# Optimization experiments

Hardware: AMD Instinct MI355X
Metric: run time of the kernel (lower is better)

The kernel has to match this reference:

```python
import jax, jax.numpy as jnp
import numpy as np
from jax import lax

B, C, H, W = 4, 64, 64, 64
CH = C // 2  # edge_detect hidden channels
BN_EPS = 1e-5


def conv1x1(x, w, b):
    # x: (B,C,H,W), w: (O,C), b: (O,)
    return jnp.einsum('bchw,oc->bohw', x, w) + b[None, :, None, None]


def setup_inputs() -> dict:
    key = jax.random.key(0)
    ks = jax.random.split(key, 12)
    s = 1.0 / np.sqrt(C)
    inp = {
        'x': jax.random.normal(ks[0], (B, C, H, W), jnp.float32),
        'Wq': jax.random.normal(ks[1], (C, C), jnp.float32) * s,
        'bq': jnp.zeros((C,), jnp.float32),
        'Wk': jax.random.normal(ks[2], (C, C), jnp.float32) * s,
        'bk': jnp.zeros((C,), jnp.float32),
        'Wv': jax.random.normal(ks[3], (C, C), jnp.float32) * s,
        'bv': jnp.zeros((C,), jnp.float32),
        'We1': jax.random.normal(ks[4], (CH, C, 3, 3), jnp.float32) * (1.0 / np.sqrt(C * 9)),
        'be1': jnp.zeros((CH,), jnp.float32),
        'bn_w': jnp.ones((CH,), jnp.float32),
        'bn_b': jnp.zeros((CH,), jnp.float32),
        'bn_mean': jnp.zeros((CH,), jnp.float32),
        'bn_var': jnp.ones((CH,), jnp.float32),
        'We2': jax.random.normal(ks[5], (1, CH), jnp.float32) * (1.0 / np.sqrt(CH)),
        'be2': jnp.zeros((1,), jnp.float32),
        'gamma': jax.random.normal(ks[6], (1,), jnp.float32) * 0.1,
        'beta': jax.random.normal(ks[7], (1,), jnp.float32) * 0.1,
    }
    return inp


def reference(x, Wq, bq, Wk, bk, Wv, bv, We1, be1, bn_w, bn_b, bn_mean, bn_var, We2, be2, gamma, beta):
    b, c, h, w = x.shape
    hw = h * w
    q = conv1x1(x, Wq, bq).reshape(b, c, hw).transpose(0, 2, 1)  # (B,HW,C)
    k = conv1x1(x, Wk, bk).reshape(b, c, hw)                      # (B,C,HW)
    v = conv1x1(x, Wv, bv).reshape(b, c, hw)                      # (B,C,HW)

    energy = jnp.einsum('bnc,bcm->bnm', q, k)                      # (B,HW,HW)
    attention = jax.nn.softmax(energy, axis=-1)

    # edge_detect: 3x3 conv -> BN (eval stats) -> ReLU -> 1x1 conv -> sigmoid
    e = lax.conv_general_dilated(x, We1, (1, 1), 'SAME',
                                 dimension_numbers=('NCHW', 'OIHW', 'NCHW'))
    e = e + be1[None, :, None, None]
    e = (e - bn_mean[None, :, None, None]) * jax.lax.rsqrt(bn_var + BN_EPS)[None, :, None, None]
    e = e * bn_w[None, :, None, None] + bn_b[None, :, None, None]
    e = jax.nn.relu(e)
    e = conv1x1(e, We2, be2)                                       # (B,1,H,W)
    edge = jax.nn.sigmoid(e).reshape(b, 1, hw)                     # (B,1,HW)

    fa = attention * (1.0 + beta[0] * edge)                        # broadcast over query dim
    denom = jnp.maximum(jnp.sum(jnp.abs(fa), axis=2, keepdims=True), 1e-12)
    fa = fa / denom                                                # L1 renorm along keys

    out = jnp.einsum('bcm,bnm->bcn', v, fa).reshape(b, c, h, w)
    return gamma[0] * out + x
```

## Files before the change

kernel.cpp:

```cpp
#include <hip/hip_runtime.h>
#include <hip/hip_bf16.h>

typedef unsigned short u16;
typedef __attribute__((ext_vector_type(8))) __bf16 bf16x8;
typedef __attribute__((ext_vector_type(4))) float f32x4;


__device__ __forceinline__ u16 f2bf(float f) {
    unsigned u = __builtin_bit_cast(unsigned, f);
    u += 0x7FFFu + ((u >> 16) & 1u);
    return (u16)(u >> 16);
}
__device__ __forceinline__ float bf2f(u16 v) {
    unsigned u = ((unsigned)v) << 16;
    return __builtin_bit_cast(float, u);
}

__global__ __launch_bounds__(256) void qkv_edge_kernel(
    const float* __restrict__ x,
    const float* __restrict__ Wq, const float* __restrict__ bq,
    const float* __restrict__ Wk, const float* __restrict__ bk,
    const float* __restrict__ Wv, const float* __restrict__ bv,
    const float* __restrict__ We1, const float* __restrict__ be1,
    const float* __restrict__ bn_w, const float* __restrict__ bn_b,
    const float* __restrict__ bn_mean, const float* __restrict__ bn_var,
    const float* __restrict__ We2, const float* __restrict__ be2,
    const float* __restrict__ beta,
    u16* __restrict__ Qt, u16* __restrict__ Kt, u16* __restrict__ Vm,
    float* __restrict__ wkey)
{
    __shared__ __align__(16) u16 sm[33280];
    const int t = threadIdx.x;
    const int wv = t >> 6, lane = t & 63;
    const int quad = lane >> 4, l15 = lane & 15;

    if (blockIdx.x < 256) {
        u16* Wl   = sm;
        u16* xt_s = sm + 13824;
        u16* vt   = sm + 13824 + 4224;
        const int b = blockIdx.x >> 6;
        const int n0 = (blockIdx.x & 63) << 6;

        const float* Wmat[3] = {Wq, Wk, Wv};
#pragma unroll
        for (int m = 0; m < 3; ++m)
#pragma unroll
            for (int i = 0; i < 4; ++i) {
                int u = t + i * 256;
                float4 w4 = *reinterpret_cast<const float4*>(Wmat[m] + u * 4);
                int row = u >> 4, col = (u & 15) * 4;
                uint2 pk;
                pk.x = (unsigned)f2bf(w4.x) | ((unsigned)f2bf(w4.y) << 16);
                pk.y = (unsigned)f2bf(w4.z) | ((unsigned)f2bf(w4.w) << 16);
                *reinterpret_cast<uint2*>(&Wl[(m * 64 + row) * 72 + col]) = pk;
            }
        for (int i = 0; i < 16; ++i) {
            int lin = t + i * 256;
            int c = lin >> 6, nn = lin & 63;
            xt_s[nn * 66 + c] = f2bf(x[(size_t)(b * 64 + c) * 4096 + n0 + nn]);
        }
        __syncthreads();

        bf16x8 bx[2];
#pragma unroll
        for (int h = 0; h < 2; ++h)
            bx[h] = *reinterpret_cast<const bf16x8*>(
                &xt_s[(wv * 16 + l15) * 66 + h * 32 + quad * 8]);

        f32x4 d[3][4];
#pragma unroll
        for (int m = 0; m < 3; ++m)
#pragma unroll
            for (int mt = 0; mt < 4; ++mt) d[m][mt] = (f32x4){0.f, 0.f, 0.f, 0.f};

#pragma unroll
        for (int h = 0; h < 2; ++h)
#pragma unroll
            for (int m = 0; m < 3; ++m)
#pragma unroll
                for (int mt = 0; mt < 4; ++mt) {
                    bf16x8 af = *reinterpret_cast<const bf16x8*>(
                        &Wl[(m * 64 + mt * 16 + l15) * 72 + h * 32 + quad * 8]);
                    d[m][mt] = __builtin_amdgcn_mfma_f32_16x16x32_bf16(af, bx[h], d[m][mt], 0, 0, 0);
                }

        const float* bias[3] = {bq, bk, bv};
        const float L2E = 1.44269504f;
#pragma unroll
        for (int m = 0; m < 3; ++m)
#pragma unroll
            for (int mt = 0; mt < 4; ++mt) {
                float4 bi = *reinterpret_cast<const float4*>(bias[m] + mt * 16 + quad * 4);
                d[m][mt][0] += bi.x; d[m][mt][1] += bi.y; d[m][mt][2] += bi.z; d[m][mt][3] += bi.w;
                if (m == 0) {
                    d[m][mt][0] *= L2E; d[m][mt][1] *= L2E;
                    d[m][mt][2] *= L2E; d[m][mt][3] *= L2E;
                }
            }

        const int rowchunk = (n0 >> 4) + wv;
#pragma unroll
        for (int m = 0; m < 2; ++m) {
            u16* base = (m == 0 ? Qt : Kt) + (size_t)b * 262144;
#pragma unroll
            for (int mt = 0; mt < 4; ++mt) {
                uint2 pk;
                pk.x = (unsigned)f2bf(d[m][mt][0]) | ((unsigned)f2bf(d[m][mt][1]) << 16);
                pk.y = (unsigned)f2bf(d[m][mt][2]) | ((unsigned)f2bf(d[m][mt][3]) << 16);
                *reinterpret_cast<uint2*>(
                    base + ((size_t)(rowchunk * 8 + mt * 2 + (quad >> 1))) * 128 +
                    l15 * 8 + (quad & 1) * 4) = pk;
            }
        }
#pragma unroll
        for (int mt = 0; mt < 4; ++mt)
#pragma unroll
            for (int r = 0; r < 4; ++r)
                vt[(mt * 16 + quad * 4 + r) * 72 + wv * 16 + l15] = f2bf(d[2][mt][r]);
        __syncthreads();
        {
            u16* Vb_st = Vm + (size_t)b * 262144;
            const int kt = n0 >> 6;
#pragma unroll
            for (int i = 0; i < 2; ++i) {
                int unit = t + i * 256;
                int f = unit >> 7, hq = (unit >> 4) & 7, cl = unit & 15;
                const u16* src = &vt[(f * 16 + cl) * 72 + hq * 8];
                uint4 v4 = *reinterpret_cast<const uint4*>(src);
                *reinterpret_cast<uint4*>(
                    Vb_st + ((size_t)((kt * 4 + f) * 8 + hq)) * 128 + cl * 8) = v4;
            }
        }
    } else {
        u16* Ae_s = sm;
        u16* xr_s = sm + 18688;
        const int eb = blockIdx.x - 256;
        const int b = eb >> 6, h = eb & 63;

        if (t < 192) {
            int kh = t / 64, rem = t & 63;
            int col = (rem >> 5) * 65, ci2 = (rem & 31) * 2;
            *reinterpret_cast<unsigned*>(&xr_s[(kh * 66 + col) * 72 + ci2]) = 0u;
        }
#pragma unroll
        for (int i = 0; i < 18; ++i) {
            int u = t + i * 256;
            int ch = u / 144;
            int rem = u - ch * 144;
            int p = rem >> 4, cig = (rem & 15) * 4;
            const float* src = We1 + ch * 576 + cig * 9 + p;
            float a = src[0], b2 = src[9], c2 = src[18], d2 = src[27];
            uint2 pk;
            pk.x = (unsigned)f2bf(a) | ((unsigned)f2bf(b2) << 16);
            pk.y = (unsigned)f2bf(c2) | ((unsigned)f2bf(d2) << 16);
            *reinterpret_cast<uint2*>(&Ae_s[ch * 584 + p * 64 + cig]) = pk;
        }
#pragma unroll
        for (int i = 0; i < 12; ++i) {
            int u = t + i * 256;
            int w = u & 63, cig = (u >> 6) & 15, kh = u >> 10;
            int hs = h + kh - 1;
            float v0 = 0.f, v1 = 0.f, v2 = 0.f, v3 = 0.f;
            if ((unsigned)hs < 64u) {
                const float* src = x + ((size_t)(b * 64 + cig * 4) * 64 + hs) * 64 + w;
                v0 = src[0]; v1 = src[4096]; v2 = src[8192]; v3 = src[12288];
            }
            uint2 pk;
            pk.x = (unsigned)f2bf(v0) | ((unsigned)f2bf(v1) << 16);
            pk.y = (unsigned)f2bf(v2) | ((unsigned)f2bf(v3) << 16);
            *reinterpret_cast<uint2*>(&xr_s[(kh * 66 + w + 1) * 72 + cig * 4]) = pk;
        }
        __syncthreads();

        f32x4 e[2];
        e[0] = (f32x4){0.f, 0.f, 0.f, 0.f};
        e[1] = (f32x4){0.f, 0.f, 0.f, 0.f};
#pragma unroll
        for (int p = 0; p < 9; ++p) {
            const int kh = p / 3, kw = p - kh * 3;
#pragma unroll
            for (int half = 0; half < 2; ++half) {
                bf16x8 bfr = *reinterpret_cast<const bf16x8*>(
                    &xr_s[(kh * 66 + wv * 16 + l15 + kw) * 72 + half * 32 + quad * 8]);
#pragma unroll
                for (int mt = 0; mt < 2; ++mt) {
                    bf16x8 af = *reinterpret_cast<const bf16x8*>(
                        &Ae_s[(mt * 16 + l15) * 584 + p * 64 + half * 32 + quad * 8]);
                    e[mt] = __builtin_amdgcn_mfma_f32_16x16x32_bf16(af, bfr, e[mt], 0, 0, 0);
                }
            }
        }
        float partial = 0.f;
#pragma unroll
        for (int mt = 0; mt < 2; ++mt) {
            float4 bw = *reinterpret_cast<const float4*>(bn_w    + mt * 16 + quad * 4);
            float4 bb = *reinterpret_cast<const float4*>(bn_b    + mt * 16 + quad * 4);
            float4 bm = *reinterpret_cast<const float4*>(bn_mean + mt * 16 + quad * 4);
            float4 bv2 = *reinterpret_cast<const float4*>(bn_var + mt * 16 + quad * 4);
            float4 b1 = *reinterpret_cast<const float4*>(be1     + mt * 16 + quad * 4);
            float4 w2 = *reinterpret_cast<const float4*>(We2     + mt * 16 + quad * 4);
            float sc, sh;
            sc = bw.x * rsqrtf(bv2.x + 1e-5f); sh = (b1.x - bm.x) * sc + bb.x;
            partial += fmaxf(e[mt][0] * sc + sh, 0.f) * w2.x;
            sc = bw.y * rsqrtf(bv2.y + 1e-5f); sh = (b1.y - bm.y) * sc + bb.y;
            partial += fmaxf(e[mt][1] * sc + sh, 0.f) * w2.y;
            sc = bw.z * rsqrtf(bv2.z + 1e-5f); sh = (b1.z - bm.z) * sc + bb.z;
            partial += fmaxf(e[mt][2] * sc + sh, 0.f) * w2.z;
            sc = bw.w * rsqrtf(bv2.w + 1e-5f); sh = (b1.w - bm.w) * sc + bb.w;
            partial += fmaxf(e[mt][3] * sc + sh, 0.f) * w2.w;
        }
        partial += __shfl_xor(partial, 16);
        partial += __shfl_xor(partial, 32);
        if (lane < 16) {
            float s = partial + be2[0];
            float sg = 1.f / (1.f + __expf(-s));
            wkey[(size_t)b * 4096 + h * 64 + wv * 16 + lane] = 1.f + beta[0] * sg;
        }
    }
}

template <int NSPLIT>
__global__ __launch_bounds__(128, 4) void attn_kernel(
    const u16* __restrict__ Qt, const u16* __restrict__ Kt,
    const u16* __restrict__ Vm, const float* __restrict__ wkey,
    u16* __restrict__ O_part, float* __restrict__ l_part)
{
    constexpr int KT_ITERS = 64 / NSPLIT;
    __shared__ __align__(16) u16 p_s_all[2 * 32 * 68];
    const int t = threadIdx.x;
    const int qi = blockIdx.x / NSPLIT;
    const int split = blockIdx.x % NSPLIT;
    const int b = qi >> 6;
    const int n0 = (qi & 63) << 6;
    const int wv = t >> 6, lane = t & 63;
    const int quad = lane >> 4, l15 = lane & 15;
    u16* p_s = p_s_all + wv * (32 * 68);

    const u16* Qb = Qt + (size_t)b * 262144;
    const u16* Kb = Kt + (size_t)b * 262144;
    const u16* Vb = Vm + (size_t)b * 262144;
    const float* wb = wkey + (size_t)b * 4096;

    bf16x8 qf[2][2];
#pragma unroll
    for (int nt = 0; nt < 2; ++nt)
#pragma unroll
        for (int h = 0; h < 2; ++h)
            qf[nt][h] = __builtin_bit_cast(bf16x8, *reinterpret_cast<const uint4*>(
                Qb + ((size_t)(((n0 >> 4) + wv * 2 + nt) * 8 + h * 4 + quad)) * 128 + l15 * 8));

    const int kt0 = split * KT_ITERS;
    uint4 kf[4][2];
    float4 wf[4];
#pragma unroll
    for (int mt = 0; mt < 4; ++mt) {
#pragma unroll
        for (int h = 0; h < 2; ++h)
            kf[mt][h] = *reinterpret_cast<const uint4*>(
                Kb + ((size_t)((kt0 * 4 + mt) * 8 + h * 4 + quad)) * 128 + l15 * 8);
        wf[mt] = *reinterpret_cast<const float4*>(wb + kt0 * 64 + mt * 16 + quad * 4);
    }

    const uint4 ones_u = {0x3F803F80u, 0x3F803F80u, 0x3F803F80u, 0x3F803F80u};
    const bf16x8 onesf = __builtin_bit_cast(bf16x8, ones_u);

    f32x4 o[2][4];
    f32x4 l5[2];
#pragma unroll
    for (int m2 = 0; m2 < 2; ++m2) {
#pragma unroll
        for (int f = 0; f < 4; ++f) o[m2][f] = (f32x4){0.f, 0.f, 0.f, 0.f};
        l5[m2] = (f32x4){0.f, 0.f, 0.f, 0.f};
    }

    for (int kt = kt0; kt < kt0 + KT_ITERS; ++kt) {
        uint4 vf[4][2];
#pragma unroll
        for (int f = 0; f < 4; ++f)
#pragma unroll
            for (int h = 0; h < 2; ++h)
                vf[f][h] = *reinterpret_cast<const uint4*>(
                    Vb + ((size_t)((kt * 4 + f) * 8 + h * 4 + quad)) * 128 + l15 * 8);

        f32x4 s[4][2];
#pragma unroll
        for (int mt = 0; mt < 4; ++mt)
#pragma unroll
            for (int nt = 0; nt < 2; ++nt) {
                f32x4 a = (f32x4){0.f, 0.f, 0.f, 0.f};
                a = __builtin_amdgcn_mfma_f32_16x16x32_bf16(
                        __builtin_bit_cast(bf16x8, kf[mt][0]), qf[nt][0], a, 0, 0, 0);
                a = __builtin_amdgcn_mfma_f32_16x16x32_bf16(
                        __builtin_bit_cast(bf16x8, kf[mt][1]), qf[nt][1], a, 0, 0, 0);
                s[mt][nt] = a;
            }

        const int ktn = (kt + 1 < kt0 + KT_ITERS) ? kt + 1 : kt0;
#pragma unroll
        for (int mt = 0; mt < 4; ++mt)
#pragma unroll
            for (int h = 0; h < 2; ++h)
                kf[mt][h] = *reinterpret_cast<const uint4*>(
                    Kb + ((size_t)((ktn * 4 + mt) * 8 + h * 4 + quad)) * 128 + l15 * 8);

        const float OFF = 17.3123405f;
#pragma unroll
        for (int mt = 0; mt < 4; ++mt) {
            const float* wfp = reinterpret_cast<const float*>(&wf[mt]);
#pragma unroll
            for (int nt = 0; nt < 2; ++nt) {
                float p0 = exp2f(s[mt][nt][0] - OFF) * wfp[0];
                float p1 = exp2f(s[mt][nt][1] - OFF) * wfp[1];
                float p2 = exp2f(s[mt][nt][2] - OFF) * wfp[2];
                float p3 = exp2f(s[mt][nt][3] - OFF) * wfp[3];
                unsigned u0 = __builtin_bit_cast(unsigned, p0);
                unsigned u1 = __builtin_bit_cast(unsigned, p1);
                unsigned u2 = __builtin_bit_cast(unsigned, p2);
                unsigned u3 = __builtin_bit_cast(unsigned, p3);
                uint2 packed;
                packed.x = (u0 >> 16) | (u1 & 0xFFFF0000u);
                packed.y = (u2 >> 16) | (u3 & 0xFFFF0000u);
                *reinterpret_cast<uint2*>(
                    &p_s[(nt * 16 + l15) * 68 + mt * 16 + quad * 4]) = packed;
            }
        }

#pragma unroll
        for (int mt = 0; mt < 4; ++mt)
            wf[mt] = *reinterpret_cast<const float4*>(wb + ktn * 64 + mt * 16 + quad * 4);

        bf16x8 pa[2][2];
#pragma unroll
        for (int m2 = 0; m2 < 2; ++m2)
#pragma unroll
            for (int h = 0; h < 2; ++h) {
                uint2 lo = *reinterpret_cast<const uint2*>(
                    &p_s[(m2 * 16 + l15) * 68 + h * 32 + quad * 8]);
                uint2 hi = *reinterpret_cast<const uint2*>(
                    &p_s[(m2 * 16 + l15) * 68 + h * 32 + quad * 8 + 4]);
                uint4 c4; c4.x = lo.x; c4.y = lo.y; c4.z = hi.x; c4.w = hi.y;
                pa[m2][h] = __builtin_bit_cast(bf16x8, c4);
            }

#pragma unroll
        for (int m2 = 0; m2 < 2; ++m2) {
#pragma unroll
            for (int f = 0; f < 4; ++f) {
                o[m2][f] = __builtin_amdgcn_mfma_f32_16x16x32_bf16(
                    pa[m2][0], __builtin_bit_cast(bf16x8, vf[f][0]), o[m2][f], 0, 0, 0);
                o[m2][f] = __builtin_amdgcn_mfma_f32_16x16x32_bf16(
                    pa[m2][1], __builtin_bit_cast(bf16x8, vf[f][1]), o[m2][f], 0, 0, 0);
            }
            l5[m2] = __builtin_amdgcn_mfma_f32_16x16x32_bf16(pa[m2][0], onesf, l5[m2], 0, 0, 0);
            l5[m2] = __builtin_amdgcn_mfma_f32_16x16x32_bf16(pa[m2][1], onesf, l5[m2], 0, 0, 0);
        }
    }

    const size_t pbase = (size_t)blockIdx.x * 4096;
#pragma unroll
    for (int m2 = 0; m2 < 2; ++m2) {
        if (l15 == 0) {
            float4 lv;
            lv.x = l5[m2][0]; lv.y = l5[m2][1]; lv.z = l5[m2][2]; lv.w = l5[m2][3];
            *reinterpret_cast<float4*>(
                &l_part[(size_t)blockIdx.x * 64 + wv * 32 + m2 * 16 + quad * 4]) = lv;
        }
#pragma unroll
        for (int f = 0; f < 4; ++f) {
            uint2 pk;
            pk.x = (unsigned)f2bf(o[m2][f][0]) | ((unsigned)f2bf(o[m2][f][1]) << 16);
            pk.y = (unsigned)f2bf(o[m2][f][2]) | ((unsigned)f2bf(o[m2][f][3]) << 16);
            *reinterpret_cast<uint2*>(
                &O_part[pbase + ((((wv * 2 + m2) * 4 + f) * 4 + quad)) * 64 + l15 * 4]) = pk;
        }
    }
}

template <int NSPLIT>
__global__ __launch_bounds__(256) void combine_kernel(
    const u16* __restrict__ O_part, const float* __restrict__ l_part,
    const float* __restrict__ x, const float* __restrict__ g_gamma,
    float* __restrict__ out)
{
    __shared__ float ot[64 * 65];
    __shared__ float ls[64];
    const int t = threadIdx.x;
    const int qi = blockIdx.x;
    const int b = qi >> 6;
    const int n0 = (qi & 63) << 6;
    const int f = t >> 6, quad = (t >> 4) & 3, l15 = t & 15;
    const float gamma = g_gamma[0];

    float acc[2][2][4];
#pragma unroll
    for (int wv = 0; wv < 2; ++wv)
#pragma unroll
        for (int m2 = 0; m2 < 2; ++m2)
#pragma unroll
            for (int r = 0; r < 4; ++r) acc[wv][m2][r] = 0.f;

#pragma unroll
    for (int s4 = 0; s4 < NSPLIT; ++s4) {
        const u16* base = O_part + ((size_t)(qi * NSPLIT + s4)) * 4096;
#pragma unroll
        for (int wv = 0; wv < 2; ++wv)
#pragma unroll
            for (int m2 = 0; m2 < 2; ++m2) {
                uint2 u = *reinterpret_cast<const uint2*>(
                    base + ((((wv * 2 + m2) * 4 + f) * 4 + quad)) * 64 + l15 * 4);
                acc[wv][m2][0] += bf2f((u16)(u.x & 0xFFFF));
                acc[wv][m2][1] += bf2f((u16)(u.x >> 16));
                acc[wv][m2][2] += bf2f((u16)(u.y & 0xFFFF));
                acc[wv][m2][3] += bf2f((u16)(u.y >> 16));
            }
    }
#pragma unroll
    for (int wv = 0; wv < 2; ++wv)
#pragma unroll
        for (int m2 = 0; m2 < 2; ++m2)
#pragma unroll
            for (int r = 0; r < 4; ++r)
                ot[(wv * 32 + m2 * 16 + quad * 4 + r) * 65 + f * 16 + l15] = acc[wv][m2][r];
    if (t < 64) {
        float lsum = 0.f;
#pragma unroll
        for (int s4 = 0; s4 < NSPLIT; ++s4)
            lsum += l_part[((size_t)(qi * NSPLIT + s4)) * 64 + t];
        ls[t] = gamma / fmaxf(lsum, 1e-30f);
    }
    __syncthreads();
    {
        const int c = t >> 2, nseg = t & 3;
        const size_t gbase = ((size_t)(b * 64 + c)) * 4096 + n0 + nseg * 16;
#pragma unroll
        for (int j = 0; j < 4; ++j) {
            float4 xv = *reinterpret_cast<const float4*>(&x[gbase + j * 4]);
            float4 rv;
            int nl = nseg * 16 + j * 4;
            rv.x = ot[(nl + 0) * 65 + c] * ls[nl + 0] + xv.x;
            rv.y = ot[(nl + 1) * 65 + c] * ls[nl + 1] + xv.y;
            rv.z = ot[(nl + 2) * 65 + c] * ls[nl + 2] + xv.z;
            rv.w = ot[(nl + 3) * 65 + c] * ls[nl + 3] + xv.w;
            *reinterpret_cast<float4*>(&out[gbase + j * 4]) = rv;
        }
    }
}

extern "C" void kernel_launch(void* const* d_in, const int* in_sizes, int n_in,
                              void* d_out, int out_size, void* d_ws, size_t ws_size,
                              hipStream_t stream) {
    const float* x      = (const float*)d_in[0];
    const float* Wq     = (const float*)d_in[1];
    const float* bq     = (const float*)d_in[2];
    const float* Wk     = (const float*)d_in[3];
    const float* bk     = (const float*)d_in[4];
    const float* Wv     = (const float*)d_in[5];
    const float* bv     = (const float*)d_in[6];
    const float* We1    = (const float*)d_in[7];
    const float* be1    = (const float*)d_in[8];
    const float* bn_w   = (const float*)d_in[9];
    const float* bn_b   = (const float*)d_in[10];
    const float* bn_mean= (const float*)d_in[11];
    const float* bn_var = (const float*)d_in[12];
    const float* We2    = (const float*)d_in[13];
    const float* be2    = (const float*)d_in[14];
    const float* gamma  = (const float*)d_in[15];
    const float* beta   = (const float*)d_in[16];

    char* ws = (char*)d_ws;
    const size_t KB = 1024, MB = 1024 * 1024;
    u16*   Qt     = (u16*)ws;
    u16*   Kt     = (u16*)(ws + 2 * MB);
    u16*   Vm     = (u16*)(ws + 4 * MB);
    float* wkey   = (float*)(ws + 6 * MB);
    float* l_part = (float*)(ws + 6 * MB + 64 * KB);
    u16*   O_part = (u16*)(ws + 6 * MB + 576 * KB);

    const bool use8 = ws_size >= (6 * MB + 576 * KB + (size_t)2048 * 64 * 64 * 2);

    float* out = (float*)d_out;

    qkv_edge_kernel<<<dim3(512), dim3(256), 0, stream>>>(
        x, Wq, bq, Wk, bk, Wv, bv, We1, be1, bn_w, bn_b, bn_mean, bn_var,
        We2, be2, beta, Qt, Kt, Vm, wkey);
    if (use8) {
        attn_kernel<8><<<dim3(2048), dim3(128), 0, stream>>>(Qt, Kt, Vm, wkey, O_part, l_part);
        combine_kernel<8><<<dim3(256), dim3(256), 0, stream>>>(O_part, l_part, x, gamma, out);
    } else {
        attn_kernel<4><<<dim3(1024), dim3(128), 0, stream>>>(Qt, Kt, Vm, wkey, O_part, l_part);
        combine_kernel<4><<<dim3(256), dim3(256), 0, stream>>>(O_part, l_part, x, gamma, out);
    }
}
```

Baseline: 148.6 us.

## Pass softmax probabilities via lane shuffles instead of LDS and transpose PV MFMA

Replaces the LDS round trip that moved the probability tile into the A-operand layout with cross-lane shuffles. The PV product is transposed so V becomes the A operand and P the B operand, which changes the accumulator layout and the row-sum output indexing. The combine kernel's shared-memory tile is adjusted to match, now written with float4 stores and a padded stride of 68. Launch bounds drop from 4 to 2 blocks per SIMD, allowing more registers but possibly lowering occupancy; the shuffles also add many cross-lane instructions per iteration.

```diff
diff --git a/kernel.cpp b/kernel.cpp
--- a/kernel.cpp
+++ b/kernel.cpp
@@ -220,13 +220,12 @@
 }
 
 template <int NSPLIT>
-__global__ __launch_bounds__(128, 4) void attn_kernel(
+__global__ __launch_bounds__(128, 2) void attn_kernel(
     const u16* __restrict__ Qt, const u16* __restrict__ Kt,
     const u16* __restrict__ Vm, const float* __restrict__ wkey,
     u16* __restrict__ O_part, float* __restrict__ l_part)
 {
     constexpr int KT_ITERS = 64 / NSPLIT;
-    __shared__ __align__(16) u16 p_s_all[2 * 32 * 68];
     const int t = threadIdx.x;
     const int qi = blockIdx.x / NSPLIT;
     const int split = blockIdx.x % NSPLIT;
@@ -234,7 +233,10 @@
     const int n0 = (qi & 63) << 6;
     const int wv = t >> 6, lane = t & 63;
     const int quad = lane >> 4, l15 = lane & 15;
-    u16* p_s = p_s_all + wv * (32 * 68);
+
+    const int src0 = ((quad & 1) * 2) * 16 + l15;
+    const int src1 = src0 + 16;
+    const bool msel = (quad >> 1) != 0;
 
     const u16* Qb = Qt + (size_t)b * 262144;
     const u16* Kb = Kt + (size_t)b * 262144;
@@ -264,14 +266,14 @@
     const uint4 ones_u = {0x3F803F80u, 0x3F803F80u, 0x3F803F80u, 0x3F803F80u};
     const bf16x8 onesf = __builtin_bit_cast(bf16x8, ones_u);
 
-    f32x4 o[2][4];
+    f32x4 o[4][2];
     f32x4 l5[2];
 #pragma unroll
-    for (int m2 = 0; m2 < 2; ++m2) {
-#pragma unroll
-        for (int f = 0; f < 4; ++f) o[m2][f] = (f32x4){0.f, 0.f, 0.f, 0.f};
-        l5[m2] = (f32x4){0.f, 0.f, 0.f, 0.f};
-    }
+    for (int fc = 0; fc < 4; ++fc)
+#pragma unroll
+        for (int nt = 0; nt < 2; ++nt) o[fc][nt] = (f32x4){0.f, 0.f, 0.f, 0.f};
+#pragma unroll
+    for (int nt = 0; nt < 2; ++nt) l5[nt] = (f32x4){0.f, 0.f, 0.f, 0.f};
 
     for (int kt = kt0; kt < kt0 + KT_ITERS; ++kt) {
         uint4 vf[4][2];
@@ -303,6 +305,7 @@
                 kf[mt][h] = *reinterpret_cast<const uint4*>(
                     Kb + ((size_t)((ktn * 4 + mt) * 8 + h * 4 + quad)) * 128 + l15 * 8);
 
+        uint2 pk[4][2];
         const float OFF = 17.3123405f;
 #pragma unroll
         for (int mt = 0; mt < 4; ++mt) {
@@ -317,11 +320,8 @@
                 unsigned u1 = __builtin_bit_cast(unsigned, p1);
                 unsigned u2 = __builtin_bit_cast(unsigned, p2);
                 unsigned u3 = __builtin_bit_cast(unsigned, p3);
-                uint2 packed;
-                packed.x = (u0 >> 16) | (u1 & 0xFFFF0000u);
-                packed.y = (u2 >> 16) | (u3 & 0xFFFF0000u);
-                *reinterpret_cast<uint2*>(
-                    &p_s[(nt * 16 + l15) * 68 + mt * 16 + quad * 4]) = packed;
+                pk[mt][nt].x = (u0 >> 16) | (u1 & 0xFFFF0000u);
+                pk[mt][nt].y = (u2 >> 16) | (u3 & 0xFFFF0000u);
             }
         }
 
@@ -329,49 +329,53 @@
         for (int mt = 0; mt < 4; ++mt)
             wf[mt] = *reinterpret_cast<const float4*>(wb + ktn * 64 + mt * 16 + quad * 4);
 
-        bf16x8 pa[2][2];
-#pragma unroll
-        for (int m2 = 0; m2 < 2; ++m2)
-#pragma unroll
-            for (int h = 0; h < 2; ++h) {
-                uint2 lo = *reinterpret_cast<const uint2*>(
-                    &p_s[(m2 * 16 + l15) * 68 + h * 32 + quad * 8]);
-                uint2 hi = *reinterpret_cast<const uint2*>(
-                    &p_s[(m2 * 16 + l15) * 68 + h * 32 + quad * 8 + 4]);
-                uint4 c4; c4.x = lo.x; c4.y = lo.y; c4.z = hi.x; c4.w = hi.y;
-                pa[m2][h] = __builtin_bit_cast(bf16x8, c4);
-            }
-
-#pragma unroll
-        for (int m2 = 0; m2 < 2; ++m2) {
-#pragma unroll
-            for (int f = 0; f < 4; ++f) {
-                o[m2][f] = __builtin_amdgcn_mfma_f32_16x16x32_bf16(
-                    pa[m2][0], __builtin_bit_cast(bf16x8, vf[f][0]), o[m2][f], 0, 0, 0);
-                o[m2][f] = __builtin_amdgcn_mfma_f32_16x16x32_bf16(
-                    pa[m2][1], __builtin_bit_cast(bf16x8, vf[f][1]), o[m2][f], 0, 0, 0);
-            }
-            l5[m2] = __builtin_amdgcn_mfma_f32_16x16x32_bf16(pa[m2][0], onesf, l5[m2], 0, 0, 0);
-            l5[m2] = __builtin_amdgcn_mfma_f32_16x16x32_bf16(pa[m2][1], onesf, l5[m2], 0, 0, 0);
+        bf16x8 pb[2][2];
+#pragma unroll
+        for (int h = 0; h < 2; ++h)
+#pragma unroll
+            for (int nt = 0; nt < 2; ++nt) {
+                unsigned a0x = (unsigned)__shfl((int)pk[h * 2][nt].x, src0, 64);
+                unsigned a1x = (unsigned)__shfl((int)pk[h * 2 + 1][nt].x, src0, 64);
+                unsigned a0y = (unsigned)__shfl((int)pk[h * 2][nt].y, src0, 64);
+                unsigned a1y = (unsigned)__shfl((int)pk[h * 2 + 1][nt].y, src0, 64);
+                unsigned a0z = (unsigned)__shfl((int)pk[h * 2][nt].x, src1, 64);
+                unsigned a1z = (unsigned)__shfl((int)pk[h * 2 + 1][nt].x, src1, 64);
+                unsigned a0w = (unsigned)__shfl((int)pk[h * 2][nt].y, src1, 64);
+                unsigned a1w = (unsigned)__shfl((int)pk[h * 2 + 1][nt].y, src1, 64);
+                uint4 g;
+                g.x = msel ? a1x : a0x;
+                g.y = msel ? a1y : a0y;
+                g.z = msel ? a1z : a0z;
+                g.w = msel ? a1w : a0w;
+                pb[nt][h] = __builtin_bit_cast(bf16x8, g);
+            }
+
+#pragma unroll
+        for (int nt = 0; nt < 2; ++nt) {
+#pragma unroll
+            for (int fc = 0; fc < 4; ++fc) {
+                o[fc][nt] = __builtin_amdgcn_mfma_f32_16x16x32_bf16(
+                    __builtin_bit_cast(bf16x8, vf[fc][0]), pb[nt][0], o[fc][nt], 0, 0, 0);
+                o[fc][nt] = __builtin_amdgcn_mfma_f32_16x16x32_bf16(
+                    __builtin_bit_cast(bf16x8, vf[fc][1]), pb[nt][1], o[fc][nt], 0, 0, 0);
+            }
+            l5[nt] = __builtin_amdgcn_mfma_f32_16x16x32_bf16(onesf, pb[nt][0], l5[nt], 0, 0, 0);
+            l5[nt] = __builtin_amdgcn_mfma_f32_16x16x32_bf16(onesf, pb[nt][1], l5[nt], 0, 0, 0);
         }
     }
 
     const size_t pbase = (size_t)blockIdx.x * 4096;
 #pragma unroll
-    for (int m2 = 0; m2 < 2; ++m2) {
-        if (l15 == 0) {
-            float4 lv;
-            lv.x = l5[m2][0]; lv.y = l5[m2][1]; lv.z = l5[m2][2]; lv.w = l5[m2][3];
-            *reinterpret_cast<float4*>(
-                &l_part[(size_t)blockIdx.x * 64 + wv * 32 + m2 * 16 + quad * 4]) = lv;
-        }
-#pragma unroll
-        for (int f = 0; f < 4; ++f) {
-            uint2 pk;
-            pk.x = (unsigned)f2bf(o[m2][f][0]) | ((unsigned)f2bf(o[m2][f][1]) << 16);
-            pk.y = (unsigned)f2bf(o[m2][f][2]) | ((unsigned)f2bf(o[m2][f][3]) << 16);
+    for (int nt = 0; nt < 2; ++nt) {
+        if (quad == 0)
+            l_part[(size_t)blockIdx.x * 64 + wv * 32 + nt * 16 + l15] = l5[nt][0];
+#pragma unroll
+        for (int fc = 0; fc < 4; ++fc) {
+            uint2 pk2;
+            pk2.x = (unsigned)f2bf(o[fc][nt][0]) | ((unsigned)f2bf(o[fc][nt][1]) << 16);
+            pk2.y = (unsigned)f2bf(o[fc][nt][2]) | ((unsigned)f2bf(o[fc][nt][3]) << 16);
             *reinterpret_cast<uint2*>(
-                &O_part[pbase + ((((wv * 2 + m2) * 4 + f) * 4 + quad)) * 64 + l15 * 4]) = pk;
+                &O_part[pbase + ((((wv * 2 + nt) * 4 + fc) * 4 + quad)) * 64 + l15 * 4]) = pk2;
         }
     }
 }
@@ -382,7 +386,7 @@
     const float* __restrict__ x, const float* __restrict__ g_gamma,
     float* __restrict__ out)
 {
-    __shared__ float ot[64 * 65];
+    __shared__ float ot[64 * 68];
     __shared__ float ls[64];
     const int t = threadIdx.x;
     const int qi = blockIdx.x;
@@ -395,9 +399,9 @@
 #pragma unroll
     for (int wv = 0; wv < 2; ++wv)
 #pragma unroll
-        for (int m2 = 0; m2 < 2; ++m2)
-#pragma unroll
-            for (int r = 0; r < 4; ++r) acc[wv][m2][r] = 0.f;
+        for (int nt = 0; nt < 2; ++nt)
+#pragma unroll
+            for (int r = 0; r < 4; ++r) acc[wv][nt][r] = 0.f;
 
 #pragma unroll
     for (int s4 = 0; s4 < NSPLIT; ++s4) {
@@ -405,22 +409,25 @@
 #pragma unroll
         for (int wv = 0; wv < 2; ++wv)
 #pragma unroll
-            for (int m2 = 0; m2 < 2; ++m2) {
+            for (int nt = 0; nt < 2; ++nt) {
                 uint2 u = *reinterpret_cast<const uint2*>(
-                    base + ((((wv * 2 + m2) * 4 + f) * 4 + quad)) * 64 + l15 * 4);
-                acc[wv][m2][0] += bf2f((u16)(u.x & 0xFFFF));
-                acc[wv][m2][1] += bf2f((u16)(u.x >> 16));
-                acc[wv][m2][2] += bf2f((u16)(u.y & 0xFFFF));
-                acc[wv][m2][3] += bf2f((u16)(u.y >> 16));
+                    base + ((((wv * 2 + nt) * 4 + f) * 4 + quad)) * 64 + l15 * 4);
+                acc[wv][nt][0] += bf2f((u16)(u.x & 0xFFFF));
+                acc[wv][nt][1] += bf2f((u16)(u.x >> 16));
+                acc[wv][nt][2] += bf2f((u16)(u.y & 0xFFFF));
+                acc[wv][nt][3] += bf2f((u16)(u.y >> 16));
             }
     }
 #pragma unroll
     for (int wv = 0; wv < 2; ++wv)
 #pragma unroll
-        for (int m2 = 0; m2 < 2; ++m2)
-#pragma unroll
-            for (int r = 0; r < 4; ++r)
-                ot[(wv * 32 + m2 * 16 + quad * 4 + r) * 65 + f * 16 + l15] = acc[wv][m2][r];
+        for (int nt = 0; nt < 2; ++nt) {
+            float4 v4;
+            v4.x = acc[wv][nt][0]; v4.y = acc[wv][nt][1];
+            v4.z = acc[wv][nt][2]; v4.w = acc[wv][nt][3];
+            *reinterpret_cast<float4*>(
+                &ot[(wv * 32 + nt * 16 + l15) * 68 + f * 16 + quad * 4]) = v4;
+        }
     if (t < 64) {
         float lsum = 0.f;
 #pragma unroll
@@ -437,10 +444,10 @@
             float4 xv = *reinterpret_cast<const float4*>(&x[gbase + j * 4]);
             float4 rv;
             int nl = nseg * 16 + j * 4;
-            rv.x = ot[(nl + 0) * 65 + c] * ls[nl + 0] + xv.x;
-            rv.y = ot[(nl + 1) * 65 + c] * ls[nl + 1] + xv.y;
-            rv.z = ot[(nl + 2) * 65 + c] * ls[nl + 2] + xv.z;
-            rv.w = ot[(nl + 3) * 65 + c] * ls[nl + 3] + xv.w;
+            rv.x = ot[(nl + 0) * 68 + c] * ls[nl + 0] + xv.x;
+            rv.y = ot[(nl + 1) * 68 + c] * ls[nl + 1] + xv.y;
+            rv.z = ot[(nl + 2) * 68 + c] * ls[nl + 2] + xv.z;
+            rv.w = ot[(nl + 3) * 68 + c] * ls[nl + 3] + xv.w;
             *reinterpret_cast<float4*>(&out[gbase + j * 4]) = rv;
         }
     }
```

Result: faster. 140.1 us (-5.7%).
